# Kernel optimization log

Measured on AMD Instinct MI355X. Metric: run time of the kernel, lower is better.

The kernel has to match this reference:

```python
import jax, jax.numpy as jnp
import numpy as np

B, T, I, H, L = 64, 512, 256, 1024, 4


def _uniform(key, shape, fan):
    # matches torch nn.RNN/Linear init: U(-1/sqrt(fan), 1/sqrt(fan))
    bound = 1.0 / np.sqrt(fan)
    return jax.random.uniform(key, shape, jnp.float32, -bound, bound)


def setup_inputs() -> dict:
    key = jax.random.key(0)
    keys = jax.random.split(key, 32)
    inp = {"x": jax.random.normal(keys[0], (B, T, I), jnp.float32)}
    k = 1
    for l in range(L):
        din = I if l == 0 else H
        inp[f"W_ih{l}"] = _uniform(keys[k], (H, din), H); k += 1
        inp[f"W_hh{l}"] = _uniform(keys[k], (H, H), H); k += 1
        inp[f"b_ih{l}"] = _uniform(keys[k], (H,), H); k += 1
        inp[f"b_hh{l}"] = _uniform(keys[k], (H,), H); k += 1
    inp["fc_w"] = _uniform(keys[k], (1, H), H); k += 1
    inp["fc_b"] = _uniform(keys[k], (1,), H)
    return inp


def _rnn_layer(x_seq, W_ih, b_ih, W_hh, b_hh):
    # x_seq: [B, T, Din] -> hidden states [B, T, H]
    # Precompute the input projection for all timesteps in one big GEMM.
    xW = jnp.einsum('btd,hd->bth', x_seq, W_ih) + b_ih  # [B, T, H]

    def step(h, xw_t):
        # h_t = tanh(W_ih x_t + b_ih + W_hh h_{t-1} + b_hh)
        h_new = jnp.tanh(xw_t + h @ W_hh.T + b_hh)
        return h_new, h_new

    h0 = jnp.zeros((x_seq.shape[0], W_hh.shape[0]), x_seq.dtype)
    _, hs = jax.lax.scan(step, h0, jnp.swapaxes(xW, 0, 1))  # [T, B, H]
    return jnp.swapaxes(hs, 0, 1)  # [B, T, H]


def reference(x,
              W_ih0, W_hh0, b_ih0, b_hh0,
              W_ih1, W_hh1, b_ih1, b_hh1,
              W_ih2, W_hh2, b_ih2, b_hh2,
              W_ih3, W_hh3, b_ih3, b_hh3,
              fc_w, fc_b):
    h = x
    layer_params = [
        (W_ih0, b_ih0, W_hh0, b_hh0),
        (W_ih1, b_ih1, W_hh1, b_hh1),
        (W_ih2, b_ih2, W_hh2, b_hh2),
        (W_ih3, b_ih3, W_hh3, b_hh3),
    ]
    for (W_ih, b_ih, W_hh, b_hh) in layer_params:
        h = _rnn_layer(h, W_ih, b_ih, W_hh, b_hh)
    return h @ fc_w.T + fc_b  # [B, T, 1]
```

## Files before the change

kernel.cpp:

```cpp
#include <hip/hip_runtime.h>


typedef _Float16 f16;
typedef _Float16 f16x8 __attribute__((ext_vector_type(8)));
typedef float    f32x4 __attribute__((ext_vector_type(4)));

#define BB 64
#define TT 512
#define II 256
#define HH 1024
#define RING 64

union U16u { unsigned long long u[2]; f16x8 v; };

#define SYS_LOAD_U64(p) __hip_atomic_load((const unsigned long long*)(p), \
    __ATOMIC_RELAXED, __HIP_MEMORY_SCOPE_SYSTEM)
#define SYS_STORE_U64(p, x) __hip_atomic_store((unsigned long long*)(p), (x), \
    __ATOMIC_RELAXED, __HIP_MEMORY_SCOPE_SYSTEM)

#define MFMA(a, b, c) __builtin_amdgcn_mfma_f32_16x16x32_f16((a), (b), (c), 0, 0, 0)

__global__ __launch_bounds__(256) void cvt_kernel(const float* __restrict__ in,
                                                  f16* __restrict__ out, int n4) {
  int stride = gridDim.x * blockDim.x;
  for (int i = blockIdx.x * blockDim.x + threadIdx.x; i < n4; i += stride) {
    float4 v = reinterpret_cast<const float4*>(in)[i];
    _Float16 __attribute__((ext_vector_type(4))) h = { (f16)v.x, (f16)v.y,
                                                       (f16)v.z, (f16)v.w };
    reinterpret_cast<decltype(h)*>(out)[i] = h;
  }
}

__global__ __launch_bounds__(256) void bsum_kernel(const float* __restrict__ a,
                                                   const float* __restrict__ b,
                                                   float* __restrict__ o) {
  int i = blockIdx.x * blockDim.x + threadIdx.x;
  if (i < HH) o[i] = a[i] + b[i];
}

__global__ __launch_bounds__(256) void zero_kernel(int* __restrict__ p, int n) {
  int i = blockIdx.x * blockDim.x + threadIdx.x;
  if (i < n) p[i] = 0;
}

__global__ __launch_bounds__(256) void initout_kernel(float* __restrict__ out,
                                                      const float* __restrict__ fcb,
                                                      int n) {
  int i = blockIdx.x * blockDim.x + threadIdx.x;
  if (i < n) out[i] = fcb[0];
}

__global__ __launch_bounds__(256, 1) void rnn_persist(
    const float* __restrict__ x,
    f16* __restrict__ ring0, f16* __restrict__ ring1,
    f16* __restrict__ ring2, f16* __restrict__ ring3,
    const f16* __restrict__ wih0, const f16* __restrict__ wih1,
    const f16* __restrict__ wih2, const f16* __restrict__ wih3,
    const f16* __restrict__ whh0, const f16* __restrict__ whh1,
    const f16* __restrict__ whh2, const f16* __restrict__ whh3,
    const float* __restrict__ bs0, const float* __restrict__ bs1,
    const float* __restrict__ bs2, const float* __restrict__ bs3,
    const float* __restrict__ fcw, float* __restrict__ out,
    int* __restrict__ flags) {
  const int p = blockIdx.x & 15, wgp = blockIdx.x >> 4;
  const int l = p >> 2, bg = p & 3;
  const int wave = threadIdx.x >> 6, lane = threadIdx.x & 63;
  const int l15 = lane & 15, quad = lane >> 4;
  const int b0 = bg * 16, r0 = wgp * 64;
  const int srow = threadIdx.x >> 4;
  const int scol = (threadIdx.x & 15) * 4;

  __shared__ f32x4 red[16 * 64];
  __shared__ __align__(16) f16 hstage[16 * 64];

  f16* rings[4] = { ring0, ring1, ring2, ring3 };
  const f16* wih_t[4] = { wih0, wih1, wih2, wih3 };
  const f16* whh_t[4] = { whh0, whh1, whh2, whh3 };
  const float* bs_t[4] = { bs0, bs1, bs2, bs3 };

  const f16* in_ring = (l > 0) ? rings[l - 1] : (const f16*)0;
  f16* out_ring = rings[l];
  const float bv = bs_t[l][r0 + wave * 16 + l15];

  f16x8 whhF[4][8];
  {
    const f16* q = whh_t[l] + (size_t)(r0 + l15) * HH + wave * 256 + quad * 8;
#pragma unroll
    for (int j = 0; j < 4; ++j)
#pragma unroll
      for (int f = 0; f < 8; ++f)
        whhF[j][f] = *reinterpret_cast<const f16x8*>(q + (size_t)j * 16 * HH + f * 32);
  }
  f16x8 wihF[4][8];
  if (l == 0) {
    const f16* q = wih_t[0] + (size_t)(r0 + l15) * II + wave * 64 + quad * 8;
#pragma unroll
    for (int j = 0; j < 4; ++j)
#pragma unroll
      for (int f = 0; f < 2; ++f)
        wihF[j][f] = *reinterpret_cast<const f16x8*>(q + (size_t)j * 16 * II + f * 32);
  } else {
    const f16* q = wih_t[l] + (size_t)(r0 + l15) * HH + wave * 256 + quad * 8;
#pragma unroll
    for (int j = 0; j < 4; ++j)
#pragma unroll
      for (int f = 0; f < 8; ++f)
        wihF[j][f] = *reinterpret_cast<const f16x8*>(q + (size_t)j * 16 * HH + f * 32);
  }
  float4 fcwv = { 0.f, 0.f, 0.f, 0.f };
  if (l == 3) fcwv = *reinterpret_cast<const float4*>(fcw + r0 + (threadIdx.x & 15) * 4);

  const int which = lane >> 4;
  int psel = p + ((which == 1) ? -4 : (which == 2) ? 4 : 0);
  psel = psel < 0 ? 0 : (psel > 15 ? 15 : psel);
  const int* fptr = flags + psel * 16 + l15;
  unsigned long long need = 0xFFFFull;
  if (l > 0) need |= 0xFFFF0000ull;
  if (l < 3) need |= 0xFFFF00000000ull;
  int* myflag = flags + p * 16 + wgp;

  for (int t = 0; t < TT; ++t) {
    const int slot = t & (RING - 1);
    f32x4 c0 = {}, c1 = {}, c2 = {}, c3 = {};

    if (l == 0) {
      const float* xp = x + ((size_t)(b0 + l15) * TT + t) * II + wave * 64 + quad * 8;
#pragma unroll
      for (int f = 0; f < 2; ++f) {
        float4 u0 = *reinterpret_cast<const float4*>(xp + f * 32);
        float4 u1 = *reinterpret_cast<const float4*>(xp + f * 32 + 4);
        f16x8 a = { (f16)u0.x, (f16)u0.y, (f16)u0.z, (f16)u0.w,
                    (f16)u1.x, (f16)u1.y, (f16)u1.z, (f16)u1.w };
        c0 = MFMA(a, wihF[0][f], c0);
        c1 = MFMA(a, wihF[1][f], c1);
        c2 = MFMA(a, wihF[2][f], c2);
        c3 = MFMA(a, wihF[3][f], c3);
      }
    }

    {
      const int tgt = (which == 0) ? t : (which == 1) ? t + 1 : t - RING + 1;
      for (;;) {
        int v = __hip_atomic_load(fptr, __ATOMIC_RELAXED, __HIP_MEMORY_SCOPE_SYSTEM);
        if ((__ballot(v >= tgt) & need) == need) break;
      }
    }

    if (l > 0) {
      const char* ip = (const char*)(in_ring + ((size_t)(b0 + l15) * RING + slot) * HH +
                                     wave * 256 + quad * 8);
#pragma unroll
      for (int f = 0; f < 8; ++f) {
        U16u av;
        av.u[0] = SYS_LOAD_U64(ip + f * 64);
        av.u[1] = SYS_LOAD_U64(ip + f * 64 + 8);
        c0 = MFMA(av.v, wihF[0][f], c0);
        c1 = MFMA(av.v, wihF[1][f], c1);
        c2 = MFMA(av.v, wihF[2][f], c2);
        c3 = MFMA(av.v, wihF[3][f], c3);
      }
    }

    if (t > 0) {
      const int slotp = (t - 1) & (RING - 1);
      const char* hp = (const char*)(out_ring + ((size_t)(b0 + l15) * RING + slotp) * HH +
                                     wave * 256 + quad * 8);
#pragma unroll
      for (int f = 0; f < 8; ++f) {
        U16u av;
        av.u[0] = SYS_LOAD_U64(hp + f * 64);
        av.u[1] = SYS_LOAD_U64(hp + f * 64 + 8);
        c0 = MFMA(av.v, whhF[0][f], c0);
        c1 = MFMA(av.v, whhF[1][f], c1);
        c2 = MFMA(av.v, whhF[2][f], c2);
        c3 = MFMA(av.v, whhF[3][f], c3);
      }
    }

    red[(wave * 4 + 0) * 64 + lane] = c0;
    red[(wave * 4 + 1) * 64 + lane] = c1;
    red[(wave * 4 + 2) * 64 + lane] = c2;
    red[(wave * 4 + 3) * 64 + lane] = c3;
    __syncthreads();
    f32x4 tot = red[(0 * 4 + wave) * 64 + lane] + red[(1 * 4 + wave) * 64 + lane] +
                red[(2 * 4 + wave) * 64 + lane] + red[(3 * 4 + wave) * 64 + lane];

#pragma unroll
    for (int i = 0; i < 4; ++i) {
      float e = __expf(2.0f * (tot[i] + bv));
      hstage[(quad * 4 + i) * 64 + wave * 16 + l15] = (f16)(1.0f - 2.0f / (e + 1.0f));
    }
    __syncthreads();

    unsigned long long hw =
        *reinterpret_cast<const unsigned long long*>(&hstage[srow * 64 + scol]);
    SYS_STORE_U64(out_ring + ((size_t)(b0 + srow) * RING + slot) * HH + r0 + scol, hw);

    if (l == 3) {
      union { unsigned long long u; f16 h[4]; } hu;
      hu.u = hw;
      float partial = (float)hu.h[0] * fcwv.x + (float)hu.h[1] * fcwv.y +
                      (float)hu.h[2] * fcwv.z + (float)hu.h[3] * fcwv.w;
      partial += __shfl_down(partial, 8, 16);
      partial += __shfl_down(partial, 4, 16);
      partial += __shfl_down(partial, 2, 16);
      partial += __shfl_down(partial, 1, 16);
      if ((threadIdx.x & 15) == 0)
        atomicAdd(out + (size_t)(b0 + srow) * TT + t, partial);
    }

    asm volatile("s_waitcnt vmcnt(0)" ::: "memory");
    __syncthreads();
    if (threadIdx.x == 0)
      __hip_atomic_store(myflag, t + 1, __ATOMIC_RELAXED, __HIP_MEMORY_SCOPE_SYSTEM);
  }
}

extern "C" void kernel_launch(void* const* d_in, const int* in_sizes, int n_in,
                              void* d_out, int out_size, void* d_ws, size_t ws_size,
                              hipStream_t stream) {
  const float* x   = (const float*)d_in[0];
  const float* fcw = (const float*)d_in[17];
  const float* fcb = (const float*)d_in[18];

  char* ws = (char*)d_ws;
  size_t off = 0;
  auto alloc = [&](size_t bytes) -> void* {
    void* p = ws + off;
    off += (bytes + 255) & ~(size_t)255;
    return p;
  };
  f16* ring[4];
  for (int l = 0; l < 4; ++l)
    ring[l] = (f16*)alloc((size_t)BB * RING * HH * 2);
  f16* w16ih[4];
  f16* w16hh[4];
  float* bsum[4];
  for (int l = 0; l < 4; ++l) {
    int din = (l == 0) ? II : HH;
    w16ih[l] = (f16*)alloc((size_t)HH * din * 2);
    w16hh[l] = (f16*)alloc((size_t)HH * HH * 2);
    bsum[l]  = (float*)alloc(HH * 4);
  }
  int* flags = (int*)alloc(256 * 4);

  for (int l = 0; l < 4; ++l) {
    int din = (l == 0) ? II : HH;
    cvt_kernel<<<512, 256, 0, stream>>>((const float*)d_in[1 + 4 * l], w16ih[l],
                                        HH * din / 4);
    cvt_kernel<<<512, 256, 0, stream>>>((const float*)d_in[2 + 4 * l], w16hh[l],
                                        HH * HH / 4);
    bsum_kernel<<<4, 256, 0, stream>>>((const float*)d_in[3 + 4 * l],
                                       (const float*)d_in[4 + 4 * l], bsum[l]);
  }
  zero_kernel<<<1, 256, 0, stream>>>(flags, 256);
  initout_kernel<<<BB * TT / 256, 256, 0, stream>>>((float*)d_out, fcb, BB * TT);

  rnn_persist<<<256, 256, 0, stream>>>(
      x, ring[0], ring[1], ring[2], ring[3],
      w16ih[0], w16ih[1], w16ih[2], w16ih[3],
      w16hh[0], w16hh[1], w16hh[2], w16hh[3],
      bsum[0], bsum[1], bsum[2], bsum[3],
      fcw, (float*)d_out, flags);
}
```

Measured before the change: 3.287 ms.

## Split flag waits into input/ring-slot and recurrence phases, pad flags to cachelines

Each progress flag is padded to its own 64-byte slot to avoid false sharing between workgroups. The single combined spin-wait is split in two. The cross-layer and ring-capacity wait happens before the input projection, and the same-layer recurrent wait happens only right before the W_hh MFMAs, so input-projection work overlaps with waiting for the previous timestep. Only wave 0 polls, and __syncthreads broadcasts readiness to the other waves, which cuts polling traffic but adds block barriers per step.

```diff
diff --git a/kernel.cpp b/kernel.cpp
--- a/kernel.cpp
+++ b/kernel.cpp
@@ -93,7 +93,7 @@
   }
   f16x8 wihF[4][8];
   if (l == 0) {
-    const f16* q = wih_t[0] + (size_t)(r0 + l15) * II + wave * 64 + quad * 8;
+    const f16* q = wih0 + (size_t)(r0 + l15) * II + wave * 64 + quad * 8;
 #pragma unroll
     for (int j = 0; j < 4; ++j)
 #pragma unroll
@@ -111,17 +111,29 @@
   if (l == 3) fcwv = *reinterpret_cast<const float4*>(fcw + r0 + (threadIdx.x & 15) * 4);
 
   const int which = lane >> 4;
-  int psel = p + ((which == 1) ? -4 : (which == 2) ? 4 : 0);
+  int psel = p + (which == 1 ? -4 : which == 2 ? 4 : 0);
   psel = psel < 0 ? 0 : (psel > 15 ? 15 : psel);
-  const int* fptr = flags + psel * 16 + l15;
-  unsigned long long need = 0xFFFFull;
-  if (l > 0) need |= 0xFFFF0000ull;
-  if (l < 3) need |= 0xFFFF00000000ull;
-  int* myflag = flags + p * 16 + wgp;
+  const int* fptr = flags + (psel * 16 + l15) * 16;
+  unsigned long long needA = 0;
+  if (l > 0) needA |= 0xFFFF0000ull;
+  if (l < 3) needA |= 0xFFFF00000000ull;
+  int* myflag = flags + (p * 16 + wgp) * 16;
 
   for (int t = 0; t < TT; ++t) {
     const int slot = t & (RING - 1);
     f32x4 c0 = {}, c1 = {}, c2 = {}, c3 = {};
+
+    if (wave == 0 && needA && (l > 0 || t >= RING)) {
+      const int tgtA = (which == 1) ? t + 1 : t - RING + 1;
+      const bool part = (which == 1 && l > 0) || (which == 2 && l < 3);
+      for (;;) {
+        int v = part ? __hip_atomic_load(fptr, __ATOMIC_RELAXED,
+                                         __HIP_MEMORY_SCOPE_SYSTEM)
+                     : 0x7FFFFFFF;
+        if ((__ballot(v >= tgtA) & needA) == needA) break;
+      }
+    }
+    if (l > 0) __syncthreads();
 
     if (l == 0) {
       const float* xp = x + ((size_t)(b0 + l15) * TT + t) * II + wave * 64 + quad * 8;
@@ -136,17 +148,7 @@
         c2 = MFMA(a, wihF[2][f], c2);
         c3 = MFMA(a, wihF[3][f], c3);
       }
-    }
-
-    {
-      const int tgt = (which == 0) ? t : (which == 1) ? t + 1 : t - RING + 1;
-      for (;;) {
-        int v = __hip_atomic_load(fptr, __ATOMIC_RELAXED, __HIP_MEMORY_SCOPE_SYSTEM);
-        if ((__ballot(v >= tgt) & need) == need) break;
-      }
-    }
-
-    if (l > 0) {
+    } else {
       const char* ip = (const char*)(in_ring + ((size_t)(b0 + l15) * RING + slot) * HH +
                                      wave * 256 + quad * 8);
 #pragma unroll
@@ -162,6 +164,16 @@
     }
 
     if (t > 0) {
+      if (wave == 0) {
+        for (;;) {
+          int v = (which == 0) ? __hip_atomic_load(fptr, __ATOMIC_RELAXED,
+                                                   __HIP_MEMORY_SCOPE_SYSTEM)
+                               : 0x7FFFFFFF;
+          if ((__ballot(v >= t) & 0xFFFFull) == 0xFFFFull) break;
+        }
+      }
+      __syncthreads();
+
       const int slotp = (t - 1) & (RING - 1);
       const char* hp = (const char*)(out_ring + ((size_t)(b0 + l15) * RING + slotp) * HH +
                                      wave * 256 + quad * 8);
@@ -242,7 +254,7 @@
     w16hh[l] = (f16*)alloc((size_t)HH * HH * 2);
     bsum[l]  = (float*)alloc(HH * 4);
   }
-  int* flags = (int*)alloc(256 * 4);
+  int* flags = (int*)alloc(256 * 16 * 4);
 
   for (int l = 0; l < 4; ++l) {
     int din = (l == 0) ? II : HH;
@@ -253,7 +265,7 @@
     bsum_kernel<<<4, 256, 0, stream>>>((const float*)d_in[3 + 4 * l],
                                        (const float*)d_in[4 + 4 * l], bsum[l]);
   }
-  zero_kernel<<<1, 256, 0, stream>>>(flags, 256);
+  zero_kernel<<<16, 256, 0, stream>>>(flags, 256 * 16);
   initout_kernel<<<BB * TT / 256, 256, 0, stream>>>((float*)d_out, fcb, BB * TT);
 
   rnn_persist<<<256, 256, 0, stream>>>(
```

Measured after the change: 3.321 ms. About the same (+1.0%).
